# Kernel tuning notes

Measured on AMD Instinct MI355X. Metric: run time of the kernel, lower is better.

Reference implementation:

```python
import jax, jax.numpy as jnp
import numpy as np

OVERLAP_THRESH = 0.5
NEG_POS_RATIO = 3
VARIANCE0 = 0.1
B, A, M = 8, 131072, 64


def point_form(boxes):
    # [.,4] cxcywh -> xyxy
    return jnp.concatenate([boxes[:, :2] - boxes[:, 2:] / 2,
                            boxes[:, :2] + boxes[:, 2:] / 2], axis=1)


def jaccard(a, b):
    # a [M,4] xyxy, b [A,4] xyxy -> IoU [M,A]
    lt = jnp.maximum(a[:, None, :2], b[None, :, :2])
    rb = jnp.minimum(a[:, None, 2:], b[None, :, 2:])
    wh = jnp.clip(rb - lt, 0.0)
    inter = wh[..., 0] * wh[..., 1]
    area_a = ((a[:, 2] - a[:, 0]) * (a[:, 3] - a[:, 1]))[:, None]
    area_b = ((b[:, 2] - b[:, 0]) * (b[:, 3] - b[:, 1]))[None, :]
    return inter / (area_a + area_b - inter)


def match_one(target, anchors_pt, anchors_c):
    # target [M,5] (xyxy, label); SSD-style bipartite + threshold matching.
    boxes = target[:, :4]
    valid = target[:, 4] > 0  # [M] padded GT rows have label 0
    num_anchors = anchors_c.shape[0]
    ov = jaccard(boxes, anchors_pt)            # [M,A]
    ov = jnp.where(valid[:, None], ov, -1.0)   # invalid GT never matches
    best_prior_idx = jnp.argmax(ov, axis=1)    # [M]
    best_truth_ov = jnp.max(ov, axis=0)        # [A]
    best_truth_idx = jnp.argmax(ov, axis=0)    # [A]
    # force each valid GT to keep its best anchor (drop updates for padded GTs)
    safe_idx = jnp.where(valid, best_prior_idx, num_anchors)
    best_truth_ov = best_truth_ov.at[safe_idx].set(2.0, mode='drop')
    best_truth_idx = best_truth_idx.at[safe_idx].set(
        jnp.arange(target.shape[0]), mode='drop')
    matched = boxes[best_truth_idx]            # [A,4]
    conf = jnp.where(best_truth_ov < OVERLAP_THRESH, 0,
                     valid[best_truth_idx].astype(jnp.int32))
    # encode: center offsets only (loc_t has 2 coords in the original)
    g_cxcy = ((matched[:, :2] + matched[:, 2:]) * 0.5 - anchors_c[:, :2]) \
             / (VARIANCE0 * anchors_c[:, 2:])
    return g_cxcy, conf


def setup_inputs() -> dict:
    key = jax.random.key(0)
    k1, k2, k3, k4, k5, k6 = jax.random.split(key, 6)
    loc_pred = jax.random.normal(k1, (B, A, 2), dtype=jnp.float32)
    conf_pred = jax.random.normal(k2, (B, A, 2), dtype=jnp.float32)
    # anchors in center form [cx,cy,w,h]
    a_cxy = jax.random.uniform(k3, (A, 2), minval=0.0, maxval=1.0)
    a_wh = jax.random.uniform(k4, (A, 2), minval=0.02, maxval=0.2)
    anchors = jnp.concatenate([a_cxy, a_wh], axis=1).astype(jnp.float32)
    # GT boxes in corner form with labels; last M//2 slots are padding (label 0)
    t_cxy = jax.random.uniform(k5, (B, M, 2), minval=0.15, maxval=0.85)
    t_wh = jax.random.uniform(k6, (B, M, 2), minval=0.05, maxval=0.25)
    t_boxes = jnp.concatenate([t_cxy - t_wh / 2, t_cxy + t_wh / 2], axis=-1)
    labels = (jnp.arange(M) < M // 2).astype(jnp.float32)
    labels = jnp.broadcast_to(labels[None, :, None], (B, M, 1))
    targets = jnp.concatenate([t_boxes, labels], axis=-1).astype(jnp.float32)
    return {"loc_pred": loc_pred, "conf_pred": conf_pred,
            "anchors": anchors, "targets": targets}


def reference(loc_pred, conf_pred, anchors, targets):
    anchors = jax.lax.stop_gradient(anchors)   # .detach() in original
    targets = jax.lax.stop_gradient(targets)
    anchors_pt = point_form(anchors)
    loc_t, conf_t = jax.vmap(match_one, in_axes=(0, None, None))(
        targets, anchors_pt, anchors)          # [B,A,2], [B,A] int
    pos = conf_t > 0                            # [B,A]
    # hard-negative mining proxy loss
    lse = jax.nn.logsumexp(conf_pred, axis=-1)  # [B,A]
    gathered = jnp.take_along_axis(conf_pred, conf_t[..., None], axis=-1)[..., 0]
    ce = lse - gathered                         # per-anchor CE (used later too)
    proxy = jnp.where(pos, 0.0, ce)
    order = jnp.argsort(-proxy, axis=1)
    rank = jnp.argsort(order, axis=1)           # rank in descending proxy order
    num_pos = jnp.sum(pos, axis=1)              # [B]
    num_neg = jnp.minimum(NEG_POS_RATIO * num_pos, pos.shape[1] - num_pos)
    neg = rank < num_neg[:, None]
    # smooth-L1 localization loss over positives (sum)
    diff = jnp.abs(loc_pred - loc_t)
    sl1 = jnp.where(diff < 1.0, 0.5 * diff * diff, diff - 0.5)
    loss_l = jnp.sum(sl1 * pos[..., None].astype(sl1.dtype))
    # cross-entropy over positives + mined negatives (sum)
    keep = (pos | neg).astype(ce.dtype)
    loss_c = jnp.sum(ce * keep)
    total_num = jnp.sum(pos).astype(loss_l.dtype)
    return loss_l / total_num, loss_c / total_num
```

## Files before the change

kernel.cpp:

```cpp
#include <hip/hip_runtime.h>
#include <cstdint>
#include <cstddef>


#define A_N 131072
#define B_N 8
#define M_N 64
#define OVTH 0.5f
#define VAR0 0.1f
#define CNT_SH 46
#define SUM_MASK ((1ull << CNT_SH) - 1ull)
#define FIXF 1048576.0f
#define INV_FIX (1.0 / 1048576.0)
#define W_BPI 16
#define W_H1  528
#define W_H2  16912
#define ZWORDS 33296
#define ZBYTES (ZWORDS * 8)

static __device__ __forceinline__ unsigned long long packCE(float ce) {
  return (1ull << CNT_SH) | (unsigned long long)(ce * FIXF + 0.5f);
}
static __device__ __forceinline__ float sl1(float d) {
  return d < 1.f ? 0.5f * d * d : d - 0.5f;
}
template <int CTRL>
static __device__ __forceinline__ float dppMax(float v) {
  int o = __builtin_amdgcn_update_dpp(0, __float_as_int(v), CTRL, 0xf, 0xf, true);
  return fmaxf(v, __int_as_float(o));
}

__launch_bounds__(512, 4)
__global__ void k_match(const float4* __restrict__ anchors,
                        const float*  __restrict__ targets,
                        const float2* __restrict__ loc_pred,
                        const float2* __restrict__ conf_pred,
                        unsigned long long* __restrict__ ws64,
                        unsigned char* __restrict__ matchOut,
                        unsigned int* __restrict__ ceBits)
{
  double* lossL  = (double*)(ws64 + 0);
  double* lossCp = (double*)(ws64 + 1);
  unsigned int* numpos = (unsigned int*)(ws64 + 2);
  unsigned long long* bpi = ws64 + W_BPI;
  unsigned long long* h1  = ws64 + W_H1;

  __shared__ float4 sTB[M_N];
  __shared__ float4 sBX[M_N];
  __shared__ float  sBA[M_N];
  __shared__ int    sBM[M_N];
  __shared__ int    sNV;
  __shared__ unsigned long long sKey[M_N][8];
  __shared__ unsigned long long hh[2048];
  __shared__ double rL[8], rC[8];
  __shared__ unsigned int rN[8];

  const int tid = threadIdx.x;
  const int wave = tid >> 6, lane = tid & 63;
  const int b = blockIdx.y;
  const int base = blockIdx.x * 2048;

  sKey[tid >> 3][tid & 7] = 0ull;
  for (int j = tid; j < 2048; j += 512) hh[j] = 0ull;
  if (tid < M_N) {
    const float* t = targets + ((size_t)b * M_N + tid) * 5;
    float x1 = t[0], y1 = t[1], x2 = t[2], y2 = t[3], lab = t[4];
    sTB[tid] = make_float4(x1, y1, x2, y2);
    bool valid = lab > 0.f;
    unsigned long long mask = __ballot(valid);
    int pfx = __popcll(mask & ((1ull << tid) - 1ull));
    if (valid) {
      sBX[pfx] = make_float4(x1, y1, x2, y2);
      sBA[pfx] = (x2 - x1) * (y2 - y1);
      sBM[pfx] = tid;
    }
    if (tid == 0) sNV = (int)__popcll(mask);
  }
  __syncthreads();

  const int nv = sNV;
  float ax1[4], ay1[4], ax2[4], ay2[4], sa[4];
  float bv[4]; int bm[4];
  #pragma unroll
  for (int i = 0; i < 4; ++i) {
    float4 an = anchors[base + tid + i * 512];
    ax1[i] = an.x - an.z * 0.5f; ay1[i] = an.y - an.w * 0.5f;
    ax2[i] = an.x + an.z * 0.5f; ay2[i] = an.y + an.w * 0.5f;
    sa[i] = (ax2[i] - ax1[i]) * (ay2[i] - ay1[i]);
    bv[i] = -1.0f; bm[i] = 0;
  }
  #pragma unroll 2
  for (int j = 0; j < nv; ++j) {
    float4 t = sBX[j];
    float ta = sBA[j];
    int mm = sBM[j];
    float lb = -1.0f; int li = 0;
    #pragma unroll
    for (int i = 0; i < 4; ++i) {
      float wx = fminf(ax2[i], t.z) - fmaxf(ax1[i], t.x);
      float wy = fminf(ay2[i], t.w) - fmaxf(ay1[i], t.y);
      float inter = fmaxf(wx, 0.f) * fmaxf(wy, 0.f);
      float uni = (sa[i] + ta) - inter;
      float q = inter * __builtin_amdgcn_rcpf(uni);
      if (q > bv[i]) { bv[i] = q; bm[i] = mm; }
      if (q > lb) { lb = q; li = i; }
    }
    float wm = lb;
    wm = dppMax<0x111>(wm);
    wm = dppMax<0x112>(wm);
    wm = dppMax<0x114>(wm);
    wm = dppMax<0x118>(wm);
    wm = dppMax<0x142>(wm);
    wm = dppMax<0x143>(wm);
    float wmax = __int_as_float(
        __builtin_amdgcn_readlane(__float_as_int(wm), 63));
    unsigned long long msk = __ballot(lb == wmax);
    int lead = __ffsll(msk) - 1;
    int wi = __builtin_amdgcn_readlane(li, lead);
    if (lane == 0) {
      int aw = base + wave * 64 + lead + wi * 512;
      sKey[mm][wave] = ((unsigned long long)__float_as_uint(wmax) << 32) |
                       (unsigned long long)(0x7FFFFFFFu - (unsigned)aw);
    }
  }

  double lL = 0.0, lC = 0.0;
  unsigned int npc = 0;
  #pragma unroll
  for (int i = 0; i < 4; ++i) {
    const int a = base + tid + i * 512;
    const size_t g = (size_t)b * A_N + a;
    bool conf = bv[i] >= OVTH;
    float2 cp = conf_pred[g];
    float mx = fmaxf(cp.x, cp.y), mn = fminf(cp.x, cp.y);
    float lse = mx + log1pf(expf(mn - mx));
    unsigned int bits = 0u;
    if (conf) {
      float ce = lse - cp.y;
      npc++; lC += (double)ce;
      float4 t = sTB[bm[i]];
      float4 an = anchors[a];
      float gx = ((t.x + t.z) * 0.5f - an.x) / (VAR0 * an.z);
      float gy = ((t.y + t.w) * 0.5f - an.y) / (VAR0 * an.w);
      float2 lp = loc_pred[g];
      lL += (double)(sl1(fabsf(lp.x - gx)) + sl1(fabsf(lp.y - gy)));
    } else {
      float ce = lse - cp.x;
      bits = __float_as_uint(ce);
      atomicAdd(&hh[bits >> 21], packCE(ce));
    }
    ceBits[g] = bits;
    matchOut[g] = (unsigned char)((conf ? 0x80 : 0) | bm[i]);
  }
  __syncthreads();

  for (int j = tid; j < 2048; j += 512) {
    unsigned long long v = hh[j];
    if (v) atomicAdd(&h1[(size_t)b * 2048 + j], v);
  }
  if (tid < M_N) {
    unsigned long long k0 = sKey[tid][0];
    #pragma unroll
    for (int w = 1; w < 8; ++w) {
      unsigned long long k2 = sKey[tid][w];
      k0 = (k2 > k0) ? k2 : k0;
    }
    if (k0) atomicMax(bpi + b * M_N + tid, k0);
  }
  for (int off = 32; off; off >>= 1) {
    lL += __shfl_down(lL, off);
    lC += __shfl_down(lC, off);
    npc += __shfl_down(npc, off);
  }
  if (lane == 0) { rL[wave] = lL; rC[wave] = lC; rN[wave] = npc; }
  __syncthreads();
  if (tid == 0) {
    double aL = 0, aC = 0; unsigned int n = 0;
    #pragma unroll
    for (int w = 0; w < 8; ++w) { aL += rL[w]; aC += rC[w]; n += rN[w]; }
    if (aL != 0.0) atomicAdd(lossL, aL);
    if (aC != 0.0) atomicAdd(lossCp, aC);
    if (n) atomicAdd(numpos + b, n);
  }
}

__launch_bounds__(512)
__global__ void k_fix(const float4* __restrict__ anchors,
                      const float*  __restrict__ targets,
                      const float2* __restrict__ loc_pred,
                      const float2* __restrict__ conf_pred,
                      unsigned long long* __restrict__ ws64,
                      const unsigned char* __restrict__ matchOut,
                      unsigned int* __restrict__ ceBits)
{
  double* lossL  = (double*)(ws64 + 0);
  double* lossCp = (double*)(ws64 + 1);
  unsigned int* numpos = (unsigned int*)(ws64 + 2);
  const unsigned long long* bpi = ws64 + W_BPI;
  unsigned long long* h1 = ws64 + W_H1;

  __shared__ int sA[512];
  __shared__ float4 sBXf[512];
  const int tid = threadIdx.x;
  const int b = tid >> 6, m = tid & 63;
  const float* t = targets + (size_t)tid * 5;
  float4 box = make_float4(t[0], t[1], t[2], t[3]);
  bool valid = t[4] > 0.f;
  unsigned long long key = bpi[tid];
  int a = valid ? (int)(0x7FFFFFFFu - (unsigned)(key & 0xFFFFFFFFull)) : -1;
  sA[tid] = a;
  sBXf[tid] = box;
  __syncthreads();
  bool winner = (a >= 0);
  if (winner) {
    for (int m2 = m + 1; m2 < M_N; ++m2)
      if (sA[(b << 6) | m2] == a) { winner = false; break; }
  }
  if (winner) {
    const size_t g = (size_t)b * A_N + a;
    unsigned char mb = matchOut[g];
    float2 cp = conf_pred[g];
    float mx = fmaxf(cp.x, cp.y), mn = fminf(cp.x, cp.y);
    float lse = mx + log1pf(expf(mn - mx));
    float4 an = anchors[a];
    float2 lp = loc_pred[g];
    float gx = ((box.x + box.z) * 0.5f - an.x) / (VAR0 * an.z);
    float gy = ((box.y + box.w) * 0.5f - an.y) / (VAR0 * an.w);
    float newL = sl1(fabsf(lp.x - gx)) + sl1(fabsf(lp.y - gy));
    if (!(mb & 0x80)) {
      float ceN = lse - cp.x;
      unsigned int bits = __float_as_uint(ceN);
      atomicAdd(&h1[(size_t)b * 2048 + (bits >> 21)],
                (unsigned long long)(0ull - packCE(ceN)));
      ceBits[g] = 0u;
      atomicAdd(lossCp, (double)(lse - cp.y));
      atomicAdd(&numpos[b], 1u);
      atomicAdd(lossL, (double)newL);
    } else {
      int oldIdx = mb & 63;
      if (oldIdx != m) {
        float4 ob = sBXf[(b << 6) | oldIdx];
        float ox = ((ob.x + ob.z) * 0.5f - an.x) / (VAR0 * an.z);
        float oy = ((ob.y + ob.w) * 0.5f - an.y) / (VAR0 * an.w);
        float oldL = sl1(fabsf(lp.x - ox)) + sl1(fabsf(lp.y - oy));
        atomicAdd(lossL, (double)(newL - oldL));
      }
    }
  }
}

template <int PER>
__device__ void findBinP(const unsigned long long* __restrict__ h,
                         unsigned int k, unsigned int* scanBuf,
                         int* outT, unsigned int* outAb)
{
  const int tid = threadIdx.x;
  unsigned int c[PER];
  unsigned int ps = 0;
  #pragma unroll
  for (int j = 0; j < PER; ++j) {
    c[j] = (unsigned int)(h[tid * PER + j] >> CNT_SH);
    ps += c[j];
  }
  scanBuf[tid] = ps;
  __syncthreads();
  unsigned int v = ps;
  for (int off = 1; off < 256; off <<= 1) {
    unsigned int u = (tid + off < 256) ? scanBuf[tid + off] : 0u;
    __syncthreads();
    v += u;
    scanBuf[tid] = v;
    __syncthreads();
  }
  unsigned int above = v - ps;
  #pragma unroll
  for (int j = PER - 1; j >= 0; --j) {
    unsigned int cj = c[j];
    if (above < k && above + cj >= k) { *outT = tid * PER + j; *outAb = above; }
    above += cj;
  }
  __syncthreads();
}

__launch_bounds__(256)
__global__ void k_sel2(const unsigned int* __restrict__ ceBits,
                       unsigned long long* __restrict__ ws64)
{
  const unsigned int* numpos = (const unsigned int*)(ws64 + 2);
  const unsigned long long* h1 = ws64 + W_H1;
  unsigned long long* h2 = ws64 + W_H2;
  __shared__ unsigned int scanBuf[256];
  __shared__ int sT; __shared__ unsigned int sAb;
  __shared__ unsigned long long hh[2048];
  const int b = blockIdx.y;
  const unsigned int P = numpos[b];
  const unsigned int k = min(3u * P, (unsigned)A_N - P);
  if (k == 0u) return;
  const int tid = threadIdx.x;
  findBinP<8>(h1 + (size_t)b * 2048, k, scanBuf, &sT, &sAb);
  const int t1 = sT;
  for (int j = tid; j < 2048; j += 256) hh[j] = 0ull;
  __syncthreads();
  const uint4* cb = (const uint4*)(ceBits + (size_t)b * A_N + blockIdx.x * 4096);
  for (int i = 0; i < 4; ++i) {
    uint4 v = cb[i * 256 + tid];
    unsigned int xs[4] = {v.x, v.y, v.z, v.w};
    #pragma unroll
    for (int c = 0; c < 4; ++c) {
      unsigned int x = xs[c];
      if (x && (int)(x >> 21) == t1)
        atomicAdd(&hh[(x >> 10) & 2047], packCE(__uint_as_float(x)));
    }
  }
  __syncthreads();
  for (int j = tid; j < 2048; j += 256) {
    unsigned long long v = hh[j];
    if (v) atomicAdd(&h2[(size_t)b * 2048 + j], v);
  }
}

__launch_bounds__(256)
__global__ void k_final(unsigned long long* __restrict__ ws64,
                        float* __restrict__ out)
{
  const double* lossL  = (const double*)(ws64 + 0);
  const double* lossCp = (const double*)(ws64 + 1);
  const unsigned int* numpos = (const unsigned int*)(ws64 + 2);
  double* lossCn = (double*)(ws64 + 6);
  unsigned int* ticket = (unsigned int*)(ws64 + 7);
  const unsigned long long* h1 = ws64 + W_H1;
  const unsigned long long* h2 = ws64 + W_H2;
  __shared__ unsigned int scanBuf[256];
  __shared__ int sT; __shared__ unsigned int sAb;
  __shared__ double lred[4];
  const int b = blockIdx.x;
  const int tid = threadIdx.x;
  const unsigned int P = numpos[b];
  const unsigned int k = min(3u * P, (unsigned)A_N - P);
  if (k > 0u) {
    findBinP<8>(h1 + (size_t)b * 2048, k, scanBuf, &sT, &sAb);
    const int t1 = sT; const unsigned int k1 = k - sAb;
    findBinP<8>(h2 + (size_t)b * 2048, k1, scanBuf, &sT, &sAb);
    const int t2 = sT; const unsigned int k2 = k1 - sAb;
    double sfix = 0.0;
    for (int j = tid; j < 2048; j += 256) {
      if (j > t1) sfix += (double)(h1[(size_t)b * 2048 + j] & SUM_MASK);
      if (j > t2) sfix += (double)(h2[(size_t)b * 2048 + j] & SUM_MASK);
    }
    double s = sfix * INV_FIX;
    const int lane = tid & 63, wave = tid >> 6;
    for (int off = 32; off; off >>= 1) s += __shfl_down(s, off);
    if (lane == 0) lred[wave] = s;
    __syncthreads();
    if (tid == 0) {
      double tot = lred[0] + lred[1] + lred[2] + lred[3];
      tot += (double)k2 * (double)__uint_as_float(
                 (((unsigned)t1 << 21) | ((unsigned)t2 << 10)));
      atomicAdd(lossCn, tot);
    }
  }
  __threadfence();
  if (tid == 0) {
    unsigned int tk = atomicAdd(ticket, 1u);
    if (tk == B_N - 1) {
      double lcn = atomicAdd(lossCn, 0.0);
      double ll = *lossL, lcp = *lossCp;
      unsigned int tot = 0;
      #pragma unroll
      for (int i = 0; i < B_N; ++i) tot += numpos[i];
      double tn = (double)tot;
      out[0] = (float)(ll / tn);
      out[1] = (float)((lcp + lcn) / tn);
    }
  }
}

extern "C" void kernel_launch(void* const* d_in, const int* in_sizes, int n_in,
                              void* d_out, int out_size, void* d_ws, size_t ws_size,
                              hipStream_t stream)
{
  const float2* loc     = (const float2*)d_in[0];
  const float2* confp   = (const float2*)d_in[1];
  const float4* anchors = (const float4*)d_in[2];
  const float*  targets = (const float*)d_in[3];
  char* ws = (char*)d_ws;
  unsigned long long* ws64 = (unsigned long long*)d_ws;
  unsigned char* matchOut = (unsigned char*)(ws + ZBYTES);
  unsigned int* ceBits = (unsigned int*)(ws + ZBYTES + 1048576);

  (void)hipMemsetAsync(d_ws, 0, ZBYTES, stream);
  k_match<<<dim3(64, 8), 512, 0, stream>>>(anchors, targets, loc, confp,
                                           ws64, matchOut, ceBits);
  k_fix<<<1, 512, 0, stream>>>(anchors, targets, loc, confp, ws64,
                               matchOut, ceBits);
  k_sel2<<<dim3(32, 8), 256, 0, stream>>>(ceBits, ws64);
  k_final<<<8, 256, 0, stream>>>(ws64, (float*)d_out);
}
```

Measured before the change: 132.0 us.

## Bin anchors spatially and cull GT boxes per block by bounding box

Adds a three-kernel counting sort that groups anchors into an 8x8 grid by center, then has each match block compute the bounding box of its anchors and test only the GT boxes that overlap it. This is meant to cut the per-anchor IoU loop from all valid GTs down to nearby candidates. The match-byte output is removed; k_fix recomputes the anchor's best GT on the fly, and ceBits is now indexed by sorted position. In exchange it adds three extra launches, scattered reads of conf and loc predictions through sortedId, and extra workspace traffic. Ties and defaults for anchors with zero overlap need care.

```diff
diff --git a/kernel.cpp b/kernel.cpp
--- a/kernel.cpp
+++ b/kernel.cpp
@@ -12,10 +12,13 @@
 #define SUM_MASK ((1ull << CNT_SH) - 1ull)
 #define FIXF 1048576.0f
 #define INV_FIX (1.0 / 1048576.0)
-#define W_BPI 16
-#define W_H1  528
-#define W_H2  16912
-#define ZWORDS 33296
+#define W_CNT 8
+#define W_CUR 40
+#define W_SP0 72
+#define W_BPI 80
+#define W_H1  592
+#define W_H2  16976
+#define ZWORDS 33360
 #define ZBYTES (ZWORDS * 8)
 
 static __device__ __forceinline__ unsigned long long packCE(float ce) {
@@ -26,17 +29,85 @@
 }
 template <int CTRL>
 static __device__ __forceinline__ float dppMax(float v) {
-  int o = __builtin_amdgcn_update_dpp(0, __float_as_int(v), CTRL, 0xf, 0xf, true);
+  int o = __builtin_amdgcn_update_dpp(__float_as_int(v), __float_as_int(v),
+                                      CTRL, 0xf, 0xf, false);
   return fmaxf(v, __int_as_float(o));
 }
+template <int CTRL>
+static __device__ __forceinline__ float dppMin(float v) {
+  int o = __builtin_amdgcn_update_dpp(__float_as_int(v), __float_as_int(v),
+                                      CTRL, 0xf, 0xf, false);
+  return fminf(v, __int_as_float(o));
+}
+static __device__ __forceinline__ float waveMax(float v) {
+  v = dppMax<0x111>(v); v = dppMax<0x112>(v); v = dppMax<0x114>(v);
+  v = dppMax<0x118>(v); v = dppMax<0x142>(v); v = dppMax<0x143>(v);
+  return __int_as_float(__builtin_amdgcn_readlane(__float_as_int(v), 63));
+}
+static __device__ __forceinline__ float waveMin(float v) {
+  v = dppMin<0x111>(v); v = dppMin<0x112>(v); v = dppMin<0x114>(v);
+  v = dppMin<0x118>(v); v = dppMin<0x142>(v); v = dppMin<0x143>(v);
+  return __int_as_float(__builtin_amdgcn_readlane(__float_as_int(v), 63));
+}
+
+__global__ void k_sort1(const float4* __restrict__ anchors,
+                        unsigned long long* __restrict__ ws64)
+{
+  unsigned int* cellCnt = (unsigned int*)(ws64 + W_CNT);
+  __shared__ unsigned int c[64];
+  const int tid = threadIdx.x;
+  if (tid < 64) c[tid] = 0u;
+  __syncthreads();
+  int gid = blockIdx.x * 256 + tid;
+  float4 an = anchors[gid];
+  int cell = min((int)(an.y * 8.f), 7) * 8 + min((int)(an.x * 8.f), 7);
+  atomicAdd(&c[cell], 1u);
+  __syncthreads();
+  if (tid < 64 && c[tid]) atomicAdd(&cellCnt[tid], c[tid]);
+}
+
+__global__ void k_sort2(unsigned long long* __restrict__ ws64)
+{
+  unsigned int* cellCnt = (unsigned int*)(ws64 + W_CNT);
+  unsigned int* cursor  = (unsigned int*)(ws64 + W_CUR);
+  if (threadIdx.x == 0) {
+    unsigned int s = 0;
+    for (int i = 0; i < 64; ++i) { cursor[i] = s; s += cellCnt[i]; }
+  }
+}
+
+__global__ void k_sort3(const float4* __restrict__ anchors,
+                        unsigned long long* __restrict__ ws64,
+                        float4* __restrict__ sortedA,
+                        unsigned int* __restrict__ sortedId)
+{
+  unsigned int* cursor  = (unsigned int*)(ws64 + W_CUR);
+  unsigned int* sortPos0 = (unsigned int*)(ws64 + W_SP0);
+  __shared__ unsigned int bcnt[64];
+  __shared__ unsigned int bbase[64];
+  const int tid = threadIdx.x;
+  if (tid < 64) bcnt[tid] = 0u;
+  __syncthreads();
+  int gid = blockIdx.x * 256 + tid;
+  float4 an = anchors[gid];
+  int cell = min((int)(an.y * 8.f), 7) * 8 + min((int)(an.x * 8.f), 7);
+  unsigned int my = atomicAdd(&bcnt[cell], 1u);
+  __syncthreads();
+  if (tid < 64) bbase[tid] = bcnt[tid] ? atomicAdd(&cursor[tid], bcnt[tid]) : 0u;
+  __syncthreads();
+  unsigned int pos = bbase[cell] + my;
+  sortedA[pos] = an;
+  sortedId[pos] = (unsigned int)gid;
+  if (gid == 0) *sortPos0 = pos;
+}
 
 __launch_bounds__(512, 4)
-__global__ void k_match(const float4* __restrict__ anchors,
+__global__ void k_match(const float4* __restrict__ sortedA,
+                        const unsigned int* __restrict__ sortedId,
                         const float*  __restrict__ targets,
                         const float2* __restrict__ loc_pred,
                         const float2* __restrict__ conf_pred,
                         unsigned long long* __restrict__ ws64,
-                        unsigned char* __restrict__ matchOut,
                         unsigned int* __restrict__ ceBits)
 {
   double* lossL  = (double*)(ws64 + 0);
@@ -46,10 +117,12 @@
   unsigned long long* h1  = ws64 + W_H1;
 
   __shared__ float4 sTB[M_N];
-  __shared__ float4 sBX[M_N];
-  __shared__ float  sBA[M_N];
-  __shared__ int    sBM[M_N];
-  __shared__ int    sNV;
+  __shared__ float4 sCBX[M_N];
+  __shared__ float  sCBA[M_N];
+  __shared__ int    sCBM[M_N];
+  __shared__ int    sNC; __shared__ int sNV; __shared__ int sFV;
+  __shared__ float  sRed[8][4];
+  __shared__ float  sBB[4];
   __shared__ unsigned long long sKey[M_N][8];
   __shared__ unsigned long long hh[2048];
   __shared__ double rL[8], rC[8];
@@ -62,38 +135,73 @@
 
   sKey[tid >> 3][tid & 7] = 0ull;
   for (int j = tid; j < 2048; j += 512) hh[j] = 0ull;
+
+  float ax1[4], ay1[4], ax2[4], ay2[4], sa[4];
+  int aId[4];
+  float bx1 = 1e30f, by1 = 1e30f, bx2 = -1e30f, by2 = -1e30f;
+  #pragma unroll
+  for (int i = 0; i < 4; ++i) {
+    const int p = base + tid + i * 512;
+    float4 an = sortedA[p];
+    aId[i] = (int)sortedId[p];
+    ax1[i] = an.x - an.z * 0.5f; ay1[i] = an.y - an.w * 0.5f;
+    ax2[i] = an.x + an.z * 0.5f; ay2[i] = an.y + an.w * 0.5f;
+    sa[i] = (ax2[i] - ax1[i]) * (ay2[i] - ay1[i]);
+    bx1 = fminf(bx1, ax1[i]); by1 = fminf(by1, ay1[i]);
+    bx2 = fmaxf(bx2, ax2[i]); by2 = fmaxf(by2, ay2[i]);
+  }
+  bx1 = waveMin(bx1); by1 = waveMin(by1);
+  bx2 = waveMax(bx2); by2 = waveMax(by2);
+  if (lane == 0) { sRed[wave][0] = bx1; sRed[wave][1] = by1;
+                   sRed[wave][2] = bx2; sRed[wave][3] = by2; }
+  __syncthreads();
+  if (tid == 0) {
+    float a0 = 1e30f, a1 = 1e30f, a2 = -1e30f, a3 = -1e30f;
+    #pragma unroll
+    for (int w = 0; w < 8; ++w) {
+      a0 = fminf(a0, sRed[w][0]); a1 = fminf(a1, sRed[w][1]);
+      a2 = fmaxf(a2, sRed[w][2]); a3 = fmaxf(a3, sRed[w][3]);
+    }
+    sBB[0] = a0; sBB[1] = a1; sBB[2] = a2; sBB[3] = a3;
+  }
+  __syncthreads();
+
   if (tid < M_N) {
     const float* t = targets + ((size_t)b * M_N + tid) * 5;
     float x1 = t[0], y1 = t[1], x2 = t[2], y2 = t[3], lab = t[4];
     sTB[tid] = make_float4(x1, y1, x2, y2);
     bool valid = lab > 0.f;
-    unsigned long long mask = __ballot(valid);
-    int pfx = __popcll(mask & ((1ull << tid) - 1ull));
-    if (valid) {
-      sBX[pfx] = make_float4(x1, y1, x2, y2);
-      sBA[pfx] = (x2 - x1) * (y2 - y1);
-      sBM[pfx] = tid;
-    }
-    if (tid == 0) sNV = (int)__popcll(mask);
-  }
-  __syncthreads();
-
-  const int nv = sNV;
-  float ax1[4], ay1[4], ax2[4], ay2[4], sa[4];
+    unsigned long long vm = __ballot(valid);
+    bool cand = valid && (x1 <= sBB[2]) && (x2 >= sBB[0]) &&
+                         (y1 <= sBB[3]) && (y2 >= sBB[1]);
+    unsigned long long cm = __ballot(cand);
+    int cp = __popcll(cm & ((1ull << tid) - 1ull));
+    if (cand) {
+      sCBX[cp] = make_float4(x1, y1, x2, y2);
+      sCBA[cp] = (x2 - x1) * (y2 - y1);
+      sCBM[cp] = tid;
+    }
+    if (tid == 0) {
+      sNC = (int)__popcll(cm);
+      sNV = (int)__popcll(vm);
+      sFV = vm ? (__ffsll(vm) - 1) : 0;
+    }
+  }
+  __syncthreads();
+
+  const int nc = sNC;
   float bv[4]; int bm[4];
-  #pragma unroll
-  for (int i = 0; i < 4; ++i) {
-    float4 an = anchors[base + tid + i * 512];
-    ax1[i] = an.x - an.z * 0.5f; ay1[i] = an.y - an.w * 0.5f;
-    ax2[i] = an.x + an.z * 0.5f; ay2[i] = an.y + an.w * 0.5f;
-    sa[i] = (ax2[i] - ax1[i]) * (ay2[i] - ay1[i]);
-    bv[i] = -1.0f; bm[i] = 0;
+  {
+    const float iv = (sNV > 0) ? 0.f : -1.0f;
+    const int im = (sNV > 0) ? sFV : 0;
+    #pragma unroll
+    for (int i = 0; i < 4; ++i) { bv[i] = iv; bm[i] = im; }
   }
   #pragma unroll 2
-  for (int j = 0; j < nv; ++j) {
-    float4 t = sBX[j];
-    float ta = sBA[j];
-    int mm = sBM[j];
+  for (int j = 0; j < nc; ++j) {
+    float4 t = sCBX[j];
+    float ta = sCBA[j];
+    int mm = sCBM[j];
     float lb = -1.0f; int li = 0;
     #pragma unroll
     for (int i = 0; i < 4; ++i) {
@@ -105,15 +213,7 @@
       if (q > bv[i]) { bv[i] = q; bm[i] = mm; }
       if (q > lb) { lb = q; li = i; }
     }
-    float wm = lb;
-    wm = dppMax<0x111>(wm);
-    wm = dppMax<0x112>(wm);
-    wm = dppMax<0x114>(wm);
-    wm = dppMax<0x118>(wm);
-    wm = dppMax<0x142>(wm);
-    wm = dppMax<0x143>(wm);
-    float wmax = __int_as_float(
-        __builtin_amdgcn_readlane(__float_as_int(wm), 63));
+    float wmax = waveMax(lb);
     unsigned long long msk = __ballot(lb == wmax);
     int lead = __ffsll(msk) - 1;
     int wi = __builtin_amdgcn_readlane(li, lead);
@@ -128,10 +228,10 @@
   unsigned int npc = 0;
   #pragma unroll
   for (int i = 0; i < 4; ++i) {
-    const int a = base + tid + i * 512;
-    const size_t g = (size_t)b * A_N + a;
+    const int p = base + tid + i * 512;
+    const size_t go = (size_t)b * A_N + aId[i];
     bool conf = bv[i] >= OVTH;
-    float2 cp = conf_pred[g];
+    float2 cp = conf_pred[go];
     float mx = fmaxf(cp.x, cp.y), mn = fminf(cp.x, cp.y);
     float lse = mx + log1pf(expf(mn - mx));
     unsigned int bits = 0u;
@@ -139,18 +239,17 @@
       float ce = lse - cp.y;
       npc++; lC += (double)ce;
       float4 t = sTB[bm[i]];
-      float4 an = anchors[a];
+      float4 an = sortedA[p];
       float gx = ((t.x + t.z) * 0.5f - an.x) / (VAR0 * an.z);
       float gy = ((t.y + t.w) * 0.5f - an.y) / (VAR0 * an.w);
-      float2 lp = loc_pred[g];
+      float2 lp = loc_pred[go];
       lL += (double)(sl1(fabsf(lp.x - gx)) + sl1(fabsf(lp.y - gy)));
     } else {
       float ce = lse - cp.x;
       bits = __float_as_uint(ce);
       atomicAdd(&hh[bits >> 21], packCE(ce));
     }
-    ceBits[g] = bits;
-    matchOut[g] = (unsigned char)((conf ? 0x80 : 0) | bm[i]);
+    ceBits[(size_t)b * A_N + p] = bits;
   }
   __syncthreads();
 
@@ -185,61 +284,89 @@
 }
 
 __launch_bounds__(512)
-__global__ void k_fix(const float4* __restrict__ anchors,
+__global__ void k_fix(const float4* __restrict__ sortedA,
+                      const unsigned int* __restrict__ sortedId,
                       const float*  __restrict__ targets,
                       const float2* __restrict__ loc_pred,
                       const float2* __restrict__ conf_pred,
                       unsigned long long* __restrict__ ws64,
-                      const unsigned char* __restrict__ matchOut,
                       unsigned int* __restrict__ ceBits)
 {
   double* lossL  = (double*)(ws64 + 0);
   double* lossCp = (double*)(ws64 + 1);
   unsigned int* numpos = (unsigned int*)(ws64 + 2);
+  const unsigned int* sortPos0 = (const unsigned int*)(ws64 + W_SP0);
   const unsigned long long* bpi = ws64 + W_BPI;
   unsigned long long* h1 = ws64 + W_H1;
 
-  __shared__ int sA[512];
+  __shared__ int sP[512];
   __shared__ float4 sBXf[512];
+  __shared__ float sAr[512];
+  __shared__ unsigned char sVal[512];
   const int tid = threadIdx.x;
   const int b = tid >> 6, m = tid & 63;
   const float* t = targets + (size_t)tid * 5;
   float4 box = make_float4(t[0], t[1], t[2], t[3]);
   bool valid = t[4] > 0.f;
+  unsigned long long vm = __ballot(valid);
+  int firstV = vm ? (__ffsll(vm) - 1) : 0;
   unsigned long long key = bpi[tid];
-  int a = valid ? (int)(0x7FFFFFFFu - (unsigned)(key & 0xFFFFFFFFull)) : -1;
-  sA[tid] = a;
+  int p = -1;
+  if (valid) {
+    unsigned int hi = (unsigned int)(key >> 32);
+    p = (hi == 0u) ? (int)*sortPos0
+                   : (int)(0x7FFFFFFFu - (unsigned)(key & 0xFFFFFFFFull));
+  }
+  sP[tid] = p;
   sBXf[tid] = box;
-  __syncthreads();
-  bool winner = (a >= 0);
+  sAr[tid] = (box.z - box.x) * (box.w - box.y);
+  sVal[tid] = valid ? 1 : 0;
+  __syncthreads();
+  bool winner = (p >= 0);
   if (winner) {
     for (int m2 = m + 1; m2 < M_N; ++m2)
-      if (sA[(b << 6) | m2] == a) { winner = false; break; }
+      if (sP[(b << 6) | m2] == p) { winner = false; break; }
   }
   if (winner) {
-    const size_t g = (size_t)b * A_N + a;
-    unsigned char mb = matchOut[g];
-    float2 cp = conf_pred[g];
+    float4 an = sortedA[p];
+    unsigned int a = sortedId[p];
+    const size_t go = (size_t)b * A_N + a;
+    float ax1 = an.x - an.z * 0.5f, ay1 = an.y - an.w * 0.5f;
+    float ax2 = an.x + an.z * 0.5f, ay2 = an.y + an.w * 0.5f;
+    float saA = (ax2 - ax1) * (ay2 - ay1);
+    float bvv = 0.f; int bmm = firstV;
+    for (int mm = 0; mm < M_N; ++mm) {
+      if (sVal[(b << 6) | mm]) {
+        float4 tb = sBXf[(b << 6) | mm];
+        float ta = sAr[(b << 6) | mm];
+        float wx = fminf(ax2, tb.z) - fmaxf(ax1, tb.x);
+        float wy = fminf(ay2, tb.w) - fmaxf(ay1, tb.y);
+        float inter = fmaxf(wx, 0.f) * fmaxf(wy, 0.f);
+        float uni = (saA + ta) - inter;
+        float q = inter * __builtin_amdgcn_rcpf(uni);
+        if (q > bvv) { bvv = q; bmm = mm; }
+      }
+    }
+    bool confOld = bvv >= OVTH;
+    float2 cp = conf_pred[go];
     float mx = fmaxf(cp.x, cp.y), mn = fminf(cp.x, cp.y);
     float lse = mx + log1pf(expf(mn - mx));
-    float4 an = anchors[a];
-    float2 lp = loc_pred[g];
+    float2 lp = loc_pred[go];
     float gx = ((box.x + box.z) * 0.5f - an.x) / (VAR0 * an.z);
     float gy = ((box.y + box.w) * 0.5f - an.y) / (VAR0 * an.w);
     float newL = sl1(fabsf(lp.x - gx)) + sl1(fabsf(lp.y - gy));
-    if (!(mb & 0x80)) {
+    if (!confOld) {
       float ceN = lse - cp.x;
       unsigned int bits = __float_as_uint(ceN);
       atomicAdd(&h1[(size_t)b * 2048 + (bits >> 21)],
                 (unsigned long long)(0ull - packCE(ceN)));
-      ceBits[g] = 0u;
+      ceBits[(size_t)b * A_N + p] = 0u;
       atomicAdd(lossCp, (double)(lse - cp.y));
       atomicAdd(&numpos[b], 1u);
       atomicAdd(lossL, (double)newL);
     } else {
-      int oldIdx = mb & 63;
-      if (oldIdx != m) {
-        float4 ob = sBXf[(b << 6) | oldIdx];
+      if (bmm != m) {
+        float4 ob = sBXf[(b << 6) | bmm];
         float ox = ((ob.x + ob.z) * 0.5f - an.x) / (VAR0 * an.z);
         float oy = ((ob.y + ob.w) * 0.5f - an.y) / (VAR0 * an.w);
         float oldL = sl1(fabsf(lp.x - ox)) + sl1(fabsf(lp.y - oy));
@@ -385,14 +512,18 @@
   const float*  targets = (const float*)d_in[3];
   char* ws = (char*)d_ws;
   unsigned long long* ws64 = (unsigned long long*)d_ws;
-  unsigned char* matchOut = (unsigned char*)(ws + ZBYTES);
-  unsigned int* ceBits = (unsigned int*)(ws + ZBYTES + 1048576);
+  float4* sortedA = (float4*)(ws + ZBYTES);
+  unsigned int* sortedId = (unsigned int*)(ws + ZBYTES + 2097152);
+  unsigned int* ceBits = (unsigned int*)(ws + ZBYTES + 2621440);
 
   (void)hipMemsetAsync(d_ws, 0, ZBYTES, stream);
-  k_match<<<dim3(64, 8), 512, 0, stream>>>(anchors, targets, loc, confp,
-                                           ws64, matchOut, ceBits);
-  k_fix<<<1, 512, 0, stream>>>(anchors, targets, loc, confp, ws64,
-                               matchOut, ceBits);
+  k_sort1<<<512, 256, 0, stream>>>(anchors, ws64);
+  k_sort2<<<1, 64, 0, stream>>>(ws64);
+  k_sort3<<<512, 256, 0, stream>>>(anchors, ws64, sortedA, sortedId);
+  k_match<<<dim3(64, 8), 512, 0, stream>>>(sortedA, sortedId, targets, loc,
+                                           confp, ws64, ceBits);
+  k_fix<<<1, 512, 0, stream>>>(sortedA, sortedId, targets, loc, confp,
+                               ws64, ceBits);
   k_sel2<<<dim3(32, 8), 256, 0, stream>>>(ceBits, ws64);
   k_final<<<8, 256, 0, stream>>>(ws64, (float*)d_out);
 }
```

Measured after the change: 147.9 us. 12.1% more time.
